# Performance work log

Measured on AMD Instinct MI355X. Metric: run time of the kernel, lower is better.

The kernel has to match this reference:

```python
import jax, jax.numpy as jnp
import numpy as np

N_LAYER = 4
N_HEAD = 16
N_EMBD = 1024
BLOCK = 1024
VOCAB = 100
TRANS = 16          # obs_dim + action_dim + 2 = 11 + 3 + 2
OBS_DIM = 11
ACT_DIM = 3
B, T = 2, 1024
VTOT = VOCAB * TRANS + 1  # token embedding rows
LN_EPS = 1e-5


def _layernorm(x, w, b):
    mu = jnp.mean(x, axis=-1, keepdims=True)
    var = jnp.var(x, axis=-1, keepdims=True)
    return (x - mu) * jax.lax.rsqrt(var + LN_EPS) * w + b


def _build_mask(t):
    # causal tril with every (joined_dim-1 mod joined_dim) column zeroed
    jd = OBS_DIM + ACT_DIM + 2  # 16
    m = jnp.tril(jnp.ones((t, t), dtype=bool))
    cols = jnp.arange(t)
    m = m & ((cols % jd) != (jd - 1))[None, :]
    return m  # [T, T] bool, True = keep


def setup_inputs() -> dict:
    key = jax.random.key(0)
    ks = jax.random.split(key, 24)
    C, L, F4 = N_EMBD, N_LAYER, 4 * N_EMBD
    g = lambda k, s: jax.random.normal(k, s, dtype=jnp.float32) * 0.02
    return {
        "tokens": jax.random.randint(ks[0], (B, T), 0, VTOT),
        "tok_emb": g(ks[1], (VTOT, C)),
        "pos_emb": g(ks[2], (1, BLOCK, C)),
        "Wq": g(ks[3], (L, C, C)), "bq": jnp.zeros((L, C), jnp.float32),
        "Wk": g(ks[4], (L, C, C)), "bk": jnp.zeros((L, C), jnp.float32),
        "Wv": g(ks[5], (L, C, C)), "bv": jnp.zeros((L, C), jnp.float32),
        "Wp": g(ks[6], (L, C, C)), "bp": jnp.zeros((L, C), jnp.float32),
        "ln1w": jnp.ones((L, C), jnp.float32), "ln1b": jnp.zeros((L, C), jnp.float32),
        "ln2w": jnp.ones((L, C), jnp.float32), "ln2b": jnp.zeros((L, C), jnp.float32),
        "W1": g(ks[7], (L, C, F4)), "b1": jnp.zeros((L, F4), jnp.float32),
        "W2": g(ks[8], (L, F4, C)), "b2": jnp.zeros((L, C), jnp.float32),
        "lnfw": jnp.ones((C,), jnp.float32), "lnfb": jnp.zeros((C,), jnp.float32),
        "head_w": g(ks[9], (TRANS, VOCAB + 1, C)),
    }


def _forward(tokens, tok_emb, pos_emb, Wq, bq, Wk, bk, Wv, bv, Wp, bp,
             ln1w, ln1b, ln2w, ln2b, W1, b1, W2, b2, lnfw, lnfb, head_w):
    b, t = tokens.shape
    C, H = N_EMBD, N_HEAD
    D = C // H
    scale = 1.0 / np.sqrt(D)
    mask = _build_mask(t)[None, None]  # [1,1,T,T]

    x = tok_emb[tokens] + pos_emb[:, :t, :]  # [B,T,C]
    for i in range(N_LAYER):
        h = _layernorm(x, ln1w[i], ln1b[i])
        q = (h @ Wq[i] + bq[i]).reshape(b, t, H, D).transpose(0, 2, 1, 3)
        k = (h @ Wk[i] + bk[i]).reshape(b, t, H, D).transpose(0, 2, 1, 3)
        v = (h @ Wv[i] + bv[i]).reshape(b, t, H, D).transpose(0, 2, 1, 3)
        att = jnp.einsum('bhtd,bhsd->bhts', q, k) * scale  # attn_bias=None => +0
        att = jnp.where(mask, att, -jnp.inf)
        att = jax.nn.softmax(att, axis=-1)
        y = jnp.einsum('bhts,bhsd->bhtd', att, v)
        y = y.transpose(0, 2, 1, 3).reshape(b, t, C)
        x = x + (y @ Wp[i] + bp[i])
        h2 = _layernorm(x, ln2w[i], ln2b[i])
        x = x + (jax.nn.gelu(h2 @ W1[i] + b1[i], approximate=False) @ W2[i] + b2[i])

    x = _layernorm(x, lnfw, lnfb)
    # pad_to_full_observation + EinLinear head
    n_pad = (TRANS - t % TRANS) % TRANS
    if n_pad:
        x = jnp.concatenate([x, jnp.zeros((b, n_pad, C), x.dtype)], axis=1)
    x_pad = x.reshape(-1, TRANS, C)                    # [b*n_states, TRANS, C]
    logits = jnp.einsum('eoi,bei->beo', head_w, x_pad)  # EinLinear, bias=False
    logits = logits.reshape(b, t + n_pad, VOCAB + 1)[:, :t]
    return logits


def reference(tokens, tok_emb, pos_emb, Wq, bq, Wk, bk, Wv, bv, Wp, bp,
              ln1w, ln1b, ln2w, ln2b, W1, b1, W2, b2, lnfw, lnfb, head_w):
    return _forward(tokens, tok_emb, pos_emb, Wq, bq, Wk, bk, Wv, bv, Wp, bp,
                    ln1w, ln1b, ln2w, ln2b, W1, b1, W2, b2, lnfw, lnfb, head_w)
```

## Files before the change

kernel.cpp:

```cpp
#include <hip/hip_runtime.h>
#include <hip/hip_bf16.h>
#include <math.h>

typedef unsigned short u16;
typedef __attribute__((ext_vector_type(8))) short short8;
typedef __attribute__((ext_vector_type(4))) float f32x4;

#define CDIM 1024
#define TDIM 1024
#define NROWS 2048
#define HEADS 16
#define HD 64
#define F4 4096

__device__ __forceinline__ u16 f2bf(float f) {
    union { float f; unsigned u; } v; v.f = f;
    unsigned r = v.u + 0x7fffu + ((v.u >> 16) & 1u);
    return (u16)(r >> 16);
}

__device__ __forceinline__ void gload_lds16(const void* g, void* lds) {
    __builtin_amdgcn_global_load_lds(
        (const __attribute__((address_space(1))) unsigned int*)g,
        (__attribute__((address_space(3))) unsigned int*)lds,
        16, 0, 0);
}

__device__ __forceinline__ void tile_map(int& bx, int& by, int& bz)
{
    const int gx = gridDim.x, gy = gridDim.y;
    const int fid = blockIdx.x + gx * (blockIdx.y + gy * blockIdx.z);
    const int nwg = gx * gy * gridDim.z;
    const int q = nwg >> 3, r = nwg & 7;
    const int xcd = fid & 7, t = fid >> 3;
    const int n = ((xcd < r) ? xcd * (q + 1) : r * (q + 1) + (xcd - r) * q) + t;
    const int nxy = gx * gy;
    bz = n / nxy;
    const int xy = n - bz * nxy;
    const int per_group = gx << 3;
    const int grp = xy / per_group;
    const int in = xy - grp * per_group;
    const int y0 = grp << 3;
    const int rem = gy - y0;
    const int gh = rem < 8 ? rem : 8;
    by = y0 + (in % gh);
    bx = in / gh;
}

__global__ __launch_bounds__(256)
void embed_k(const int* __restrict__ tok, const float* __restrict__ te,
             const float* __restrict__ pe, float* __restrict__ X)
{
    const int row = blockIdx.x;
    const int t = row & (TDIM - 1);
    const int tk = tok[row];
    const int c = threadIdx.x * 4;
    float4 a = *reinterpret_cast<const float4*>(te + (size_t)tk * CDIM + c);
    float4 b = *reinterpret_cast<const float4*>(pe + (size_t)t * CDIM + c);
    a.x += b.x; a.y += b.y; a.z += b.z; a.w += b.w;
    *reinterpret_cast<float4*>(X + (size_t)row * CDIM + c) = a;
}

template<bool BF16OUT>
__global__ __launch_bounds__(256)
void ln_k(const float* __restrict__ X, const float* __restrict__ g,
          const float* __restrict__ be, void* __restrict__ outp)
{
    __shared__ float red[4], red2[4];
    const int row = blockIdx.x, tid = threadIdx.x;
    const float* xr = X + (size_t)row * CDIM;
    const int c = tid * 4;
    float4 xv = *reinterpret_cast<const float4*>(xr + c);
    float s  = xv.x + xv.y + xv.z + xv.w;
    float s2 = xv.x*xv.x + xv.y*xv.y + xv.z*xv.z + xv.w*xv.w;
    #pragma unroll
    for (int off = 32; off; off >>= 1) {
        s  += __shfl_xor(s, off);
        s2 += __shfl_xor(s2, off);
    }
    if ((tid & 63) == 0) { red[tid >> 6] = s; red2[tid >> 6] = s2; }
    __syncthreads();
    const float ts  = red[0] + red[1] + red[2] + red[3];
    const float ts2 = red2[0] + red2[1] + red2[2] + red2[3];
    const float mu  = ts * (1.0f / CDIM);
    const float var = ts2 * (1.0f / CDIM) - mu * mu;
    const float rs  = rsqrtf(var + 1e-5f);
    float4 gv = *reinterpret_cast<const float4*>(g + c);
    float4 bv = *reinterpret_cast<const float4*>(be + c);
    float o0 = (xv.x - mu) * rs * gv.x + bv.x;
    float o1 = (xv.y - mu) * rs * gv.y + bv.y;
    float o2 = (xv.z - mu) * rs * gv.z + bv.z;
    float o3 = (xv.w - mu) * rs * gv.w + bv.w;
    if (BF16OUT) {
        u16 tmp[4] = { f2bf(o0), f2bf(o1), f2bf(o2), f2bf(o3) };
        u16* o = (u16*)outp + (size_t)row * CDIM + c;
        *reinterpret_cast<uint2*>(o) = *reinterpret_cast<const uint2*>(tmp);
    } else {
        float4 ov = { o0, o1, o2, o3 };
        *reinterpret_cast<float4*>((float*)outp + (size_t)row * CDIM + c) = ov;
    }
}

template<bool BF16OUT, int NZ>
__global__ __launch_bounds__(256)
void ln_red_k(float* __restrict__ X, const float* __restrict__ P,
              const float* __restrict__ g, const float* __restrict__ be,
              void* __restrict__ outp)
{
    __shared__ float red[4], red2[4];
    const int row = blockIdx.x, tid = threadIdx.x;
    const int c = tid * 4;
    float4 xv = *reinterpret_cast<const float4*>(X + (size_t)row * CDIM + c);
    #pragma unroll
    for (int z = 0; z < NZ; ++z) {
        float4 pv = *reinterpret_cast<const float4*>(P + ((size_t)z * NROWS + row) * CDIM + c);
        xv.x += pv.x; xv.y += pv.y; xv.z += pv.z; xv.w += pv.w;
    }
    *reinterpret_cast<float4*>(X + (size_t)row * CDIM + c) = xv;
    float s  = xv.x + xv.y + xv.z + xv.w;
    float s2 = xv.x*xv.x + xv.y*xv.y + xv.z*xv.z + xv.w*xv.w;
    #pragma unroll
    for (int off = 32; off; off >>= 1) {
        s  += __shfl_xor(s, off);
        s2 += __shfl_xor(s2, off);
    }
    if ((tid & 63) == 0) { red[tid >> 6] = s; red2[tid >> 6] = s2; }
    __syncthreads();
    const float ts  = red[0] + red[1] + red[2] + red[3];
    const float ts2 = red2[0] + red2[1] + red2[2] + red2[3];
    const float mu  = ts * (1.0f / CDIM);
    const float var = ts2 * (1.0f / CDIM) - mu * mu;
    const float rs  = rsqrtf(var + 1e-5f);
    float4 gv = *reinterpret_cast<const float4*>(g + c);
    float4 bv = *reinterpret_cast<const float4*>(be + c);
    float o0 = (xv.x - mu) * rs * gv.x + bv.x;
    float o1 = (xv.y - mu) * rs * gv.y + bv.y;
    float o2 = (xv.z - mu) * rs * gv.z + bv.z;
    float o3 = (xv.w - mu) * rs * gv.w + bv.w;
    if (BF16OUT) {
        u16 tmp[4] = { f2bf(o0), f2bf(o1), f2bf(o2), f2bf(o3) };
        u16* o = (u16*)outp + (size_t)row * CDIM + c;
        *reinterpret_cast<uint2*>(o) = *reinterpret_cast<const uint2*>(tmp);
    } else {
        float4 ov = { o0, o1, o2, o3 };
        *reinterpret_cast<float4*>((float*)outp + (size_t)row * CDIM + c) = ov;
    }
}

__global__ __launch_bounds__(256)
void convT_k(const float* __restrict__ W, u16* __restrict__ Wt,
             const int K, const int N)
{
    __shared__ u16 s[64][72];
    const int k0 = blockIdx.y * 64, n0 = blockIdx.x * 64;
    const int tr = threadIdx.x >> 4, tc = (threadIdx.x & 15) * 4;
    #pragma unroll
    for (int i = 0; i < 4; ++i) {
        int r = tr + i * 16;
        float4 w = *reinterpret_cast<const float4*>(W + (size_t)(k0 + r) * N + n0 + tc);
        s[r][tc + 0] = f2bf(w.x); s[r][tc + 1] = f2bf(w.y);
        s[r][tc + 2] = f2bf(w.z); s[r][tc + 3] = f2bf(w.w);
    }
    __syncthreads();
    #pragma unroll
    for (int i = 0; i < 4; ++i) {
        int n = tr + i * 16;
        u16 tmp[4];
        #pragma unroll
        for (int e = 0; e < 4; ++e) tmp[e] = s[tc + e][n];
        *reinterpret_cast<uint2*>(Wt + (size_t)(n0 + n) * K + k0 + tc) =
            *reinterpret_cast<const uint2*>(tmp);
    }
}

__global__ __launch_bounds__(256)
void pack_bias_k(const float* __restrict__ a, const float* __restrict__ b,
                 const float* __restrict__ c, float* __restrict__ o)
{
    const int i = threadIdx.x * 4;
    const float* s = blockIdx.x == 0 ? a : blockIdx.x == 1 ? b : c;
    *reinterpret_cast<float4*>(o + (size_t)blockIdx.x * 1024 + i) =
        *reinterpret_cast<const float4*>(s + i);
}

template<int EPI>
__global__ __launch_bounds__(256, 2)
void gemm_bt(const u16* __restrict__ A, const u16* __restrict__ Bt,
             const float* __restrict__ bias, u16* __restrict__ outb,
             float* __restrict__ resid, u16* __restrict__ vtout,
             const int N, const int K, const int KCH)
{
    __shared__ __align__(16) u16 sA[2][2][128 * 32];
    __shared__ __align__(16) u16 sB[2][2][128 * 32];
    const int tid = threadIdx.x;
    const int lane = tid & 63, wv = tid >> 6;
    int bx, by, bz;
    tile_map(bx, by, bz);
    const int m0 = by * 128, n0 = bx * 128;
    const int kbeg = bz * KCH, kend = kbeg + KCH;
    const int fr = lane & 15, fq = lane >> 4;
    const int wm = wv & 1, wn = wv >> 1;
    const int srow = lane >> 2, schunk = (lane & 3) * 8;
    f32x4 acc[4][4] = {};

    auto stage = [&](int k0, int buf) {
        #pragma unroll
        for (int kk = 0; kk < 2; ++kk)
            #pragma unroll
            for (int i = 0; i < 2; ++i) {
                const int reg = i * 4 + wv;
                gload_lds16(A  + (size_t)(m0 + reg * 16 + srow) * K + k0 + kk * 32 + schunk,
                            &sA[buf][kk][reg * 512]);
                gload_lds16(Bt + (size_t)(n0 + reg * 16 + srow) * K + k0 + kk * 32 + schunk,
                            &sB[buf][kk][reg * 512]);
            }
    };

    stage(kbeg, 0);
    int cur = 0;
    for (int k0 = kbeg; k0 < kend; k0 += 64) {
        __syncthreads();
        if (k0 + 64 < kend) stage(k0 + 64, cur ^ 1);
        #pragma unroll
        for (int kk = 0; kk < 2; ++kk) {
            short8 af[4], bf[4];
            #pragma unroll
            for (int mi = 0; mi < 4; ++mi)
                af[mi] = *reinterpret_cast<const short8*>(
                    &sA[cur][kk][(wm * 64 + mi * 16 + fr) * 32 + fq * 8]);
            #pragma unroll
            for (int nj = 0; nj < 4; ++nj)
                bf[nj] = *reinterpret_cast<const short8*>(
                    &sB[cur][kk][(wn * 64 + nj * 16 + fr) * 32 + fq * 8]);
            #pragma unroll
            for (int mi = 0; mi < 4; ++mi)
                #pragma unroll
                for (int nj = 0; nj < 4; ++nj)
                    acc[mi][nj] = __builtin_amdgcn_mfma_f32_16x16x32_bf16(af[mi], bf[nj], acc[mi][nj], 0, 0, 0);
        }
        cur ^= 1;
    }

    #pragma unroll
    for (int nj = 0; nj < 4; ++nj) {
        const int col = n0 + wn * 64 + nj * 16 + fr;
        const float bias_v = (EPI == 2 && bz != 0) ? 0.0f : bias[col];
        #pragma unroll
        for (int mi = 0; mi < 4; ++mi) {
            const int rowb = m0 + wm * 64 + mi * 16 + fq * 4;
            if (EPI == 0 && vtout != nullptr && col >= 2048) {
                const int bidx = rowb >> 10, t = rowb & 1023, hd = col - 2048;
                u16 t4[4];
                #pragma unroll
                for (int r = 0; r < 4; ++r) t4[r] = f2bf(acc[mi][nj][r] + bias_v);
                *reinterpret_cast<uint2*>(
                    vtout + ((size_t)(bidx * 16 + (hd >> 6)) * 64 + (hd & 63)) * 1024 + t) =
                    *reinterpret_cast<const uint2*>(t4);
            } else {
                #pragma unroll
                for (int r = 0; r < 4; ++r) {
                    const int row = rowb + r;
                    float cv = acc[mi][nj][r] + bias_v;
                    if (EPI == 0) {
                        outb[(size_t)row * N + col] = f2bf(cv);
                    } else if (EPI == 1) {
                        float gl = 0.5f * cv * (1.0f + erff(cv * 0.70710678118654752f));
                        outb[(size_t)row * N + col] = f2bf(gl);
                    } else {
                        resid[((size_t)bz * NROWS + row) * N + col] = cv;
                    }
                }
            }
        }
    }
}

__global__ __launch_bounds__(256)
void attn_k(const u16* __restrict__ QKV, const u16* __restrict__ VT,
            u16* __restrict__ Y)
{
    __shared__ __align__(16) u16 sQ[64][72];
    __shared__ __align__(16) u16 sK[2][64][72];
    __shared__ __align__(16) u16 sV[2][64][72];
    __shared__ __align__(16) u16 sP[64][72];
    const int tid = threadIdx.x, lane = tid & 63, wv = tid >> 6;
    const int fr = lane & 15, fq = lane >> 4;
    int bx, by, bz;
    tile_map(bx, by, bz);
    const int qt = gridDim.x - 1 - bx;
    const int h = by, b = bz, q0 = qt * 64;
    const u16* Qb = QKV + (size_t)b * TDIM * 3072 + h * HD;
    const u16* Vb = VT + ((size_t)(b * HEADS + h) * HD) * TDIM;
    const int r0 = tid >> 3, c0 = (tid & 7) * 8;

    #pragma unroll
    for (int i = 0; i < 2; ++i) {
        const int r = r0 + i * 32;
        *reinterpret_cast<uint4*>(&sQ[r][c0]) =
            *reinterpret_cast<const uint4*>(Qb + (size_t)(q0 + r) * 3072 + c0);
        *reinterpret_cast<uint4*>(&sK[0][r][c0]) =
            *reinterpret_cast<const uint4*>(Qb + 1024 + (size_t)r * 3072 + c0);
        *reinterpret_cast<uint4*>(&sV[0][r][c0]) =
            *reinterpret_cast<const uint4*>(Vb + (size_t)r * TDIM + c0);
    }
    __syncthreads();

    short8 ones;
    #pragma unroll
    for (int e = 0; e < 8; ++e) ones[e] = (short)0x3F80;

    short8 aQ0 = *reinterpret_cast<const short8*>(&sQ[wv * 16 + fr][fq * 8]);
    short8 aQ1 = *reinterpret_cast<const short8*>(&sQ[wv * 16 + fr][32 + fq * 8]);
    f32x4 o[4] = {};
    f32x4 osum = {};

    for (int st = 0; st <= qt; ++st) {
        const int cur = st & 1, s0 = st * 64;
        const bool pf = st < qt;
        uint4 pk[2], pv[2];
        if (pf) {
            #pragma unroll
            for (int i = 0; i < 2; ++i) {
                const int r = r0 + i * 32;
                pk[i] = *reinterpret_cast<const uint4*>(Qb + 1024 + (size_t)(s0 + 64 + r) * 3072 + c0);
                pv[i] = *reinterpret_cast<const uint4*>(Vb + (size_t)r * TDIM + s0 + 64 + c0);
            }
        }
        f32x4 sacc[4] = {};
        #pragma unroll
        for (int j = 0; j < 4; ++j) {
            short8 b0 = *reinterpret_cast<const short8*>(&sK[cur][j * 16 + fr][fq * 8]);
            sacc[j] = __builtin_amdgcn_mfma_f32_16x16x32_bf16(aQ0, b0, sacc[j], 0, 0, 0);
            short8 b1 = *reinterpret_cast<const short8*>(&sK[cur][j * 16 + fr][32 + fq * 8]);
            sacc[j] = __builtin_amdgcn_mfma_f32_16x16x32_bf16(aQ1, b1, sacc[j], 0, 0, 0);
        }
        #pragma unroll
        for (int j = 0; j < 4; ++j)
            #pragma unroll
            for (int r = 0; r < 4; ++r) {
                const int qrow = q0 + wv * 16 + fq * 4 + r;
                const int scol = s0 + j * 16 + fr;
                const bool keep = (scol <= qrow) && ((scol & 15) != 15);
                const float p = keep ? __expf(sacc[j][r] * 0.125f) : 0.0f;
                sP[wv * 16 + fq * 4 + r][j * 16 + fr] = f2bf(p);
            }
        short8 aP0 = *reinterpret_cast<const short8*>(&sP[wv * 16 + fr][fq * 8]);
        short8 aP1 = *reinterpret_cast<const short8*>(&sP[wv * 16 + fr][32 + fq * 8]);
        #pragma unroll
        for (int j = 0; j < 4; ++j) {
            short8 b0 = *reinterpret_cast<const short8*>(&sV[cur][j * 16 + fr][fq * 8]);
            o[j] = __builtin_amdgcn_mfma_f32_16x16x32_bf16(aP0, b0, o[j], 0, 0, 0);
            short8 b1 = *reinterpret_cast<const short8*>(&sV[cur][j * 16 + fr][32 + fq * 8]);
            o[j] = __builtin_amdgcn_mfma_f32_16x16x32_bf16(aP1, b1, o[j], 0, 0, 0);
        }
        osum = __builtin_amdgcn_mfma_f32_16x16x32_bf16(aP0, ones, osum, 0, 0, 0);
        osum = __builtin_amdgcn_mfma_f32_16x16x32_bf16(aP1, ones, osum, 0, 0, 0);
        if (pf) {
            #pragma unroll
            for (int i = 0; i < 2; ++i) {
                const int r = r0 + i * 32;
                *reinterpret_cast<uint4*>(&sK[cur ^ 1][r][c0]) = pk[i];
                *reinterpret_cast<uint4*>(&sV[cur ^ 1][r][c0]) = pv[i];
            }
        }
        __syncthreads();
    }

    float rcp[4];
    #pragma unroll
    for (int r = 0; r < 4; ++r) rcp[r] = 1.0f / osum[r];
    const size_t ybase = ((size_t)b * TDIM + q0) * CDIM + h * HD;
    #pragma unroll
    for (int j = 0; j < 4; ++j)
        #pragma unroll
        for (int r = 0; r < 4; ++r) {
            const int row = wv * 16 + fq * 4 + r, col = j * 16 + fr;
            Y[ybase + (size_t)row * CDIM + col] = f2bf(o[j][r] * rcp[r]);
        }
}

__global__ __launch_bounds__(256)
void head_k(const float* __restrict__ Xf, const float* __restrict__ HW,
             float* __restrict__ out)
{
    const int row = blockIdx.x;
    const int e = row & 15;
    const float* xr = Xf + (size_t)row * CDIM;
    const float* wbase = HW + (size_t)e * 101 * CDIM;
    const int lane = threadIdx.x & 63, wv = threadIdx.x >> 6;
    for (int o = wv; o < 101; o += 4) {
        const float* wr = wbase + (size_t)o * CDIM;
        float s = 0.0f;
        #pragma unroll
        for (int i = 0; i < CDIM / 64; ++i)
            s += xr[lane + i * 64] * wr[lane + i * 64];
        #pragma unroll
        for (int off = 32; off; off >>= 1) s += __shfl_xor(s, off);
        if (lane == 0) out[(size_t)row * 101 + o] = s;
    }
}

extern "C" void kernel_launch(void* const* d_in, const int* in_sizes, int n_in,
                              void* d_out, int out_size, void* d_ws, size_t ws_size,
                              hipStream_t stream)
{
    const int*   tokens = (const int*)  d_in[0];
    const float* tok_emb= (const float*)d_in[1];
    const float* pos_emb= (const float*)d_in[2];
    const float* Wq = (const float*)d_in[3];
    const float* bq = (const float*)d_in[4];
    const float* Wk = (const float*)d_in[5];
    const float* bk = (const float*)d_in[6];
    const float* Wv = (const float*)d_in[7];
    const float* bv = (const float*)d_in[8];
    const float* Wp = (const float*)d_in[9];
    const float* bp = (const float*)d_in[10];
    const float* ln1w = (const float*)d_in[11];
    const float* ln1b = (const float*)d_in[12];
    const float* ln2w = (const float*)d_in[13];
    const float* ln2b = (const float*)d_in[14];
    const float* W1 = (const float*)d_in[15];
    const float* b1 = (const float*)d_in[16];
    const float* W2 = (const float*)d_in[17];
    const float* b2 = (const float*)d_in[18];
    const float* lnfw = (const float*)d_in[19];
    const float* lnfb = (const float*)d_in[20];
    const float* head_w = (const float*)d_in[21];
    float* out = (float*)d_out;

    char* ws = (char*)d_ws;
    float* x    = (float*)(ws);
    u16*   hbuf = (u16*)  (ws + (8u  << 20));
    u16*   yb   = (u16*)  (ws + (8u  << 20));
    u16*   qkv  = (u16*)  (ws + (12u << 20));
    u16*   vt   = (u16*)  (ws + (24u << 20));
    u16*   mid  = (u16*)  (ws + (12u << 20));
    float* hf   = (float*)(ws + (12u << 20));
    u16*   wbuf = (u16*)  (ws + (28u << 20));
    float* pbuf = (float*)(ws + (36u << 20));
    float* bbuf = (float*)(ws + (68u << 20));

    embed_k<<<NROWS, 256, 0, stream>>>(tokens, tok_emb, pos_emb, x);

    for (int l = 0; l < 4; ++l) {
        const size_t wo = (size_t)l * CDIM * CDIM;
        convT_k<<<dim3(16, 16), 256, 0, stream>>>(Wq + wo, wbuf + 0u * CDIM * CDIM, CDIM, CDIM);
        convT_k<<<dim3(16, 16), 256, 0, stream>>>(Wk + wo, wbuf + 1u * CDIM * CDIM, CDIM, CDIM);
        convT_k<<<dim3(16, 16), 256, 0, stream>>>(Wv + wo, wbuf + 2u * CDIM * CDIM, CDIM, CDIM);
        pack_bias_k<<<3, 256, 0, stream>>>(bq + l * CDIM, bk + l * CDIM, bv + l * CDIM, bbuf);

        if (l == 0)
            ln_k<true><<<NROWS, 256, 0, stream>>>(x, ln1w, ln1b, hbuf);
        else
            ln_red_k<true, 4><<<NROWS, 256, 0, stream>>>(x, pbuf, ln1w + l * CDIM, ln1b + l * CDIM, hbuf);
        gemm_bt<0><<<dim3(24, 16, 1), 256, 0, stream>>>(hbuf, wbuf, bbuf, qkv, nullptr, vt, 3072, CDIM, CDIM);
        attn_k<<<dim3(16, HEADS, 2), 256, 0, stream>>>(qkv, vt, yb);

        convT_k<<<dim3(16, 16), 256, 0, stream>>>(Wp + wo, wbuf, CDIM, CDIM);
        gemm_bt<2><<<dim3(8, 16, 2), 256, 0, stream>>>(yb, wbuf, bp + l * CDIM, nullptr, pbuf, nullptr, CDIM, CDIM, 512);

        ln_red_k<true, 2><<<NROWS, 256, 0, stream>>>(x, pbuf, ln2w + l * CDIM, ln2b + l * CDIM, hbuf);
        convT_k<<<dim3(64, 16), 256, 0, stream>>>(W1 + (size_t)l * CDIM * F4, wbuf, CDIM, F4);
        gemm_bt<1><<<dim3(32, 16, 1), 256, 0, stream>>>(hbuf, wbuf, b1 + l * F4, mid, nullptr, nullptr, F4, CDIM, CDIM);
        convT_k<<<dim3(16, 64), 256, 0, stream>>>(W2 + (size_t)l * F4 * CDIM, wbuf, F4, CDIM);
        gemm_bt<2><<<dim3(8, 16, 4), 256, 0, stream>>>(mid, wbuf, b2 + l * CDIM, nullptr, pbuf, nullptr, CDIM, F4, CDIM);
    }

    ln_red_k<false, 4><<<NROWS, 256, 0, stream>>>(x, pbuf, lnfw, lnfb, hf);
    head_k<<<NROWS, 256, 0, stream>>>(hf, head_w, out);
}
```

Before: 984.7 us.

## Split attention KV range across two blocks, keep P in registers, retile head

Attention now splits each query tile's key range into two halves processed by separate blocks (split-K). Each block writes unnormalized partial outputs and row sums, and a new combine kernel adds them and normalizes. The kernel also computes S transposed so P stays in registers, which removes the sP LDS round trip and the ones-MFMA row sum. The head kernel is restructured so each wave keeps its x row in registers, reuses it across two weight rows per iteration, and uses float4 loads. The cost is an extra launch and fp32 partial traffic through the workspace.

New measurement: 980.9 us. Within noise of the previous version (-0.4%).

```diff
diff --git a/kernel.cpp b/kernel.cpp
--- a/kernel.cpp
+++ b/kernel.cpp
@@ -4,6 +4,7 @@
 
 typedef unsigned short u16;
 typedef __attribute__((ext_vector_type(8))) short short8;
+typedef __attribute__((ext_vector_type(4))) short short4v;
 typedef __attribute__((ext_vector_type(4))) float f32x4;
 
 #define CDIM 1024
@@ -17,6 +18,9 @@
     union { float f; unsigned u; } v; v.f = f;
     unsigned r = v.u + 0x7fffu + ((v.u >> 16) & 1u);
     return (u16)(r >> 16);
+}
+__device__ __forceinline__ float bf2f(u16 h) {
+    union { unsigned u; float f; } v; v.u = (unsigned)h << 16; return v.f;
 }
 
 __device__ __forceinline__ void gload_lds16(const void* g, void* lds) {
@@ -275,48 +279,47 @@
     }
 }
 
-__global__ __launch_bounds__(256)
+__global__ __launch_bounds__(256, 4)
 void attn_k(const u16* __restrict__ QKV, const u16* __restrict__ VT,
-            u16* __restrict__ Y)
-{
-    __shared__ __align__(16) u16 sQ[64][72];
+            float* __restrict__ po, float* __restrict__ plsum)
+{
     __shared__ __align__(16) u16 sK[2][64][72];
     __shared__ __align__(16) u16 sV[2][64][72];
-    __shared__ __align__(16) u16 sP[64][72];
     const int tid = threadIdx.x, lane = tid & 63, wv = tid >> 6;
     const int fr = lane & 15, fq = lane >> 4;
     int bx, by, bz;
     tile_map(bx, by, bz);
-    const int qt = gridDim.x - 1 - bx;
-    const int h = by, b = bz, q0 = qt * 64;
+    const int qt = bx, h = by, b = bz >> 1, sc = bz & 1;
+    const int q0 = qt * 64;
+    const int nt = qt + 1, h1 = (nt + 1) >> 1;
+    const int stbeg = sc ? h1 : 0, stend = sc ? nt : h1;
     const u16* Qb = QKV + (size_t)b * TDIM * 3072 + h * HD;
     const u16* Vb = VT + ((size_t)(b * HEADS + h) * HD) * TDIM;
     const int r0 = tid >> 3, c0 = (tid & 7) * 8;
 
-    #pragma unroll
-    for (int i = 0; i < 2; ++i) {
-        const int r = r0 + i * 32;
-        *reinterpret_cast<uint4*>(&sQ[r][c0]) =
-            *reinterpret_cast<const uint4*>(Qb + (size_t)(q0 + r) * 3072 + c0);
-        *reinterpret_cast<uint4*>(&sK[0][r][c0]) =
-            *reinterpret_cast<const uint4*>(Qb + 1024 + (size_t)r * 3072 + c0);
-        *reinterpret_cast<uint4*>(&sV[0][r][c0]) =
-            *reinterpret_cast<const uint4*>(Vb + (size_t)r * TDIM + c0);
-    }
-    __syncthreads();
-
-    short8 ones;
-    #pragma unroll
-    for (int e = 0; e < 8; ++e) ones[e] = (short)0x3F80;
-
-    short8 aQ0 = *reinterpret_cast<const short8*>(&sQ[wv * 16 + fr][fq * 8]);
-    short8 aQ1 = *reinterpret_cast<const short8*>(&sQ[wv * 16 + fr][32 + fq * 8]);
+    const u16* qp = Qb + (size_t)(q0 + wv * 16 + fr) * 3072 + fq * 8;
+    short8 aQ0 = *reinterpret_cast<const short8*>(qp);
+    short8 aQ1 = *reinterpret_cast<const short8*>(qp + 32);
+
     f32x4 o[4] = {};
-    f32x4 osum = {};
-
-    for (int st = 0; st <= qt; ++st) {
-        const int cur = st & 1, s0 = st * 64;
-        const bool pf = st < qt;
+    float lsum = 0.0f;
+    int cur = 0;
+
+    if (stbeg < stend) {
+        #pragma unroll
+        for (int i = 0; i < 2; ++i) {
+            const int r = r0 + i * 32;
+            *reinterpret_cast<uint4*>(&sK[0][r][c0]) =
+                *reinterpret_cast<const uint4*>(Qb + 1024 + (size_t)(stbeg * 64 + r) * 3072 + c0);
+            *reinterpret_cast<uint4*>(&sV[0][r][c0]) =
+                *reinterpret_cast<const uint4*>(Vb + (size_t)r * TDIM + stbeg * 64 + c0);
+        }
+        __syncthreads();
+    }
+
+    for (int st = stbeg; st < stend; ++st) {
+        const int s0 = st * 64;
+        const bool pf = (st + 1) < stend;
         uint4 pk[2], pv[2];
         if (pf) {
             #pragma unroll
@@ -329,32 +332,45 @@
         f32x4 sacc[4] = {};
         #pragma unroll
         for (int j = 0; j < 4; ++j) {
-            short8 b0 = *reinterpret_cast<const short8*>(&sK[cur][j * 16 + fr][fq * 8]);
-            sacc[j] = __builtin_amdgcn_mfma_f32_16x16x32_bf16(aQ0, b0, sacc[j], 0, 0, 0);
-            short8 b1 = *reinterpret_cast<const short8*>(&sK[cur][j * 16 + fr][32 + fq * 8]);
-            sacc[j] = __builtin_amdgcn_mfma_f32_16x16x32_bf16(aQ1, b1, sacc[j], 0, 0, 0);
-        }
+            short8 k0f = *reinterpret_cast<const short8*>(&sK[cur][j * 16 + fr][fq * 8]);
+            sacc[j] = __builtin_amdgcn_mfma_f32_16x16x32_bf16(k0f, aQ0, sacc[j], 0, 0, 0);
+            short8 k1f = *reinterpret_cast<const short8*>(&sK[cur][j * 16 + fr][32 + fq * 8]);
+            sacc[j] = __builtin_amdgcn_mfma_f32_16x16x32_bf16(k1f, aQ1, sacc[j], 0, 0, 0);
+        }
+        const int qrow = q0 + wv * 16 + fr;
+        u16 pb[4][4];
         #pragma unroll
         for (int j = 0; j < 4; ++j)
             #pragma unroll
             for (int r = 0; r < 4; ++r) {
-                const int qrow = q0 + wv * 16 + fq * 4 + r;
-                const int scol = s0 + j * 16 + fr;
+                const int scol = s0 + j * 16 + fq * 4 + r;
                 const bool keep = (scol <= qrow) && ((scol & 15) != 15);
                 const float p = keep ? __expf(sacc[j][r] * 0.125f) : 0.0f;
-                sP[wv * 16 + fq * 4 + r][j * 16 + fr] = f2bf(p);
+                const u16 hb = f2bf(p);
+                pb[j][r] = hb;
+                lsum += bf2f(hb);
             }
-        short8 aP0 = *reinterpret_cast<const short8*>(&sP[wv * 16 + fr][fq * 8]);
-        short8 aP1 = *reinterpret_cast<const short8*>(&sP[wv * 16 + fr][32 + fq * 8]);
+        union { unsigned u[4]; short8 v; } a0, a1;
+        a0.u[0] = (unsigned)pb[0][0] | ((unsigned)pb[0][1] << 16);
+        a0.u[1] = (unsigned)pb[0][2] | ((unsigned)pb[0][3] << 16);
+        a0.u[2] = (unsigned)pb[1][0] | ((unsigned)pb[1][1] << 16);
+        a0.u[3] = (unsigned)pb[1][2] | ((unsigned)pb[1][3] << 16);
+        a1.u[0] = (unsigned)pb[2][0] | ((unsigned)pb[2][1] << 16);
+        a1.u[1] = (unsigned)pb[2][2] | ((unsigned)pb[2][3] << 16);
+        a1.u[2] = (unsigned)pb[3][0] | ((unsigned)pb[3][1] << 16);
+        a1.u[3] = (unsigned)pb[3][2] | ((unsigned)pb[3][3] << 16);
         #pragma unroll
         for (int j = 0; j < 4; ++j) {
-            short8 b0 = *reinterpret_cast<const short8*>(&sV[cur][j * 16 + fr][fq * 8]);
-            o[j] = __builtin_amdgcn_mfma_f32_16x16x32_bf16(aP0, b0, o[j], 0, 0, 0);
-            short8 b1 = *reinterpret_cast<const short8*>(&sV[cur][j * 16 + fr][32 + fq * 8]);
-            o[j] = __builtin_amdgcn_mfma_f32_16x16x32_bf16(aP1, b1, o[j], 0, 0, 0);
-        }
-        osum = __builtin_amdgcn_mfma_f32_16x16x32_bf16(aP0, ones, osum, 0, 0, 0);
-        osum = __builtin_amdgcn_mfma_f32_16x16x32_bf16(aP1, ones, osum, 0, 0, 0);
+            const u16* vrow = &sV[cur][j * 16 + fr][0];
+            short4v v0 = *reinterpret_cast<const short4v*>(vrow + fq * 4);
+            short4v v1 = *reinterpret_cast<const short4v*>(vrow + 16 + fq * 4);
+            short8 bV0 = __builtin_shufflevector(v0, v1, 0, 1, 2, 3, 4, 5, 6, 7);
+            o[j] = __builtin_amdgcn_mfma_f32_16x16x32_bf16(a0.v, bV0, o[j], 0, 0, 0);
+            short4v v2 = *reinterpret_cast<const short4v*>(vrow + 32 + fq * 4);
+            short4v v3 = *reinterpret_cast<const short4v*>(vrow + 48 + fq * 4);
+            short8 bV1 = __builtin_shufflevector(v2, v3, 0, 1, 2, 3, 4, 5, 6, 7);
+            o[j] = __builtin_amdgcn_mfma_f32_16x16x32_bf16(a1.v, bV1, o[j], 0, 0, 0);
+        }
         if (pf) {
             #pragma unroll
             for (int i = 0; i < 2; ++i) {
@@ -362,41 +378,88 @@
                 *reinterpret_cast<uint4*>(&sK[cur ^ 1][r][c0]) = pk[i];
                 *reinterpret_cast<uint4*>(&sV[cur ^ 1][r][c0]) = pv[i];
             }
-        }
-        __syncthreads();
-    }
-
-    float rcp[4];
-    #pragma unroll
-    for (int r = 0; r < 4; ++r) rcp[r] = 1.0f / osum[r];
-    const size_t ybase = ((size_t)b * TDIM + q0) * CDIM + h * HD;
+            __syncthreads();
+            cur ^= 1;
+        }
+    }
+
+    lsum += __shfl_xor(lsum, 16);
+    lsum += __shfl_xor(lsum, 32);
+
+    const int tl = (bz * 16 + h) * 16 + qt;
+    float* pt = po + (size_t)tl * 4096;
     #pragma unroll
     for (int j = 0; j < 4; ++j)
         #pragma unroll
-        for (int r = 0; r < 4; ++r) {
-            const int row = wv * 16 + fq * 4 + r, col = j * 16 + fr;
-            Y[ybase + (size_t)row * CDIM + col] = f2bf(o[j][r] * rcp[r]);
-        }
+        for (int r = 0; r < 4; ++r)
+            pt[(wv * 16 + fq * 4 + r) * 64 + j * 16 + fr] = o[j][r];
+    if (fq == 0) plsum[(size_t)tl * 64 + wv * 16 + fr] = lsum;
+}
+
+__global__ __launch_bounds__(256)
+void attn_comb_k(const float* __restrict__ po, const float* __restrict__ plsum,
+                 u16* __restrict__ Y)
+{
+    const int qt = blockIdx.x, h = blockIdx.y, b = blockIdx.z;
+    const int t0 = ((b * 2 + 0) * 16 + h) * 16 + qt;
+    const int t1 = ((b * 2 + 1) * 16 + h) * 16 + qt;
+    const float* p0 = po + (size_t)t0 * 4096;
+    const float* p1 = po + (size_t)t1 * 4096;
+    const float* l0 = plsum + (size_t)t0 * 64;
+    const float* l1 = plsum + (size_t)t1 * 64;
+    #pragma unroll
+    for (int i = 0; i < 4; ++i) {
+        const int f4 = threadIdx.x + i * 256;
+        const int q = f4 >> 4, d4 = (f4 & 15) * 4;
+        float4 a = *reinterpret_cast<const float4*>(p0 + f4 * 4);
+        float4 c = *reinterpret_cast<const float4*>(p1 + f4 * 4);
+        const float rl = 1.0f / (l0[q] + l1[q]);
+        u16 t4[4] = { f2bf((a.x + c.x) * rl), f2bf((a.y + c.y) * rl),
+                      f2bf((a.z + c.z) * rl), f2bf((a.w + c.w) * rl) };
+        *reinterpret_cast<uint2*>(
+            Y + ((size_t)(b * TDIM + qt * 64 + q)) * CDIM + h * HD + d4) =
+            *reinterpret_cast<const uint2*>(t4);
+    }
 }
 
 __global__ __launch_bounds__(256)
 void head_k(const float* __restrict__ Xf, const float* __restrict__ HW,
-             float* __restrict__ out)
-{
-    const int row = blockIdx.x;
-    const int e = row & 15;
-    const float* xr = Xf + (size_t)row * CDIM;
-    const float* wbase = HW + (size_t)e * 101 * CDIM;
-    const int lane = threadIdx.x & 63, wv = threadIdx.x >> 6;
-    for (int o = wv; o < 101; o += 4) {
-        const float* wr = wbase + (size_t)o * CDIM;
-        float s = 0.0f;
-        #pragma unroll
-        for (int i = 0; i < CDIM / 64; ++i)
-            s += xr[lane + i * 64] * wr[lane + i * 64];
-        #pragma unroll
-        for (int off = 32; off; off >>= 1) s += __shfl_xor(s, off);
-        if (lane == 0) out[(size_t)row * 101 + o] = s;
+            float* __restrict__ out)
+{
+    int bx, by, bz;
+    tile_map(bx, by, bz);
+    const int e = by, b = bz;
+    const int lane = threadIdx.x & 63, w = threadIdx.x >> 6;
+    const int p = e + 16 * (bx * 4 + w);
+    const size_t rowi = (size_t)b * 1024 + p;
+    const float* xr = Xf + rowi * CDIM;
+    float4 xa[4];
+    #pragma unroll
+    for (int i = 0; i < 4; ++i)
+        xa[i] = *reinterpret_cast<const float4*>(xr + lane * 4 + i * 256);
+    const float* wb = HW + (size_t)e * 101 * CDIM;
+    float* orow = out + rowi * 101;
+    for (int o = 0; o < 101; o += 2) {
+        const int o2 = o + 1 < 101 ? o + 1 : 100;
+        const float* wr0 = wb + (size_t)o * CDIM;
+        const float* wr1 = wb + (size_t)o2 * CDIM;
+        float s0 = 0.0f, s1 = 0.0f;
+        #pragma unroll
+        for (int i = 0; i < 4; ++i) {
+            float4 w0 = *reinterpret_cast<const float4*>(wr0 + lane * 4 + i * 256);
+            float4 w1 = *reinterpret_cast<const float4*>(wr1 + lane * 4 + i * 256);
+            s0 += xa[i].x * w0.x + xa[i].y * w0.y + xa[i].z * w0.z + xa[i].w * w0.w;
+            s1 += xa[i].x * w1.x + xa[i].y * w1.y + xa[i].z * w1.z + xa[i].w * w1.w;
+        }
+        #pragma unroll
+        for (int off = 32; off; off >>= 1) {
+            s0 += __shfl_xor(s0, off);
+            s1 += __shfl_xor(s1, off);
+        }
+        if (lane == 0) {
+            orow[o] = s0;
+            if (o + 1 < 101) orow[o + 1] = s1;
+        }
     }
 }
 
@@ -438,6 +501,8 @@
     float* hf   = (float*)(ws + (12u << 20));
     u16*   wbuf = (u16*)  (ws + (28u << 20));
     float* pbuf = (float*)(ws + (36u << 20));
+    float* po   = (float*)(ws + (36u << 20));
+    float* plsum= (float*)(ws + (53u << 20));
     float* bbuf = (float*)(ws + (68u << 20));
 
     embed_k<<<NROWS, 256, 0, stream>>>(tokens, tok_emb, pos_emb, x);
@@ -454,7 +519,8 @@
         else
             ln_red_k<true, 4><<<NROWS, 256, 0, stream>>>(x, pbuf, ln1w + l * CDIM, ln1b + l * CDIM, hbuf);
         gemm_bt<0><<<dim3(24, 16, 1), 256, 0, stream>>>(hbuf, wbuf, bbuf, qkv, nullptr, vt, 3072, CDIM, CDIM);
-        attn_k<<<dim3(16, HEADS, 2), 256, 0, stream>>>(qkv, vt, yb);
+        attn_k<<<dim3(16, HEADS, 4), 256, 0, stream>>>(qkv, vt, po, plsum);
+        attn_comb_k<<<dim3(16, HEADS, 2), 256, 0, stream>>>(po, plsum, yb);
 
         convT_k<<<dim3(16, 16), 256, 0, stream>>>(Wp + wo, wbuf, CDIM, CDIM);
         gemm_bt<2><<<dim3(8, 16, 2), 256, 0, stream>>>(yb, wbuf, bp + l * CDIM, nullptr, pbuf, nullptr, CDIM, CDIM, 512);
@@ -467,5 +533,5 @@
     }
 
     ln_red_k<false, 4><<<NROWS, 256, 0, stream>>>(x, pbuf, lnfw, lnfb, hf);
-    head_k<<<NROWS, 256, 0, stream>>>(hf, head_w, out);
-}
+    head_k<<<dim3(16, 16, 2), 256, 0, stream>>>(hf, head_w, out);
+}
```
